# Kernel optimization log

Measured on AMD Instinct MI355X. Metric: run time of the kernel, lower is better.

## Reference

```python
import jax, jax.numpy as jnp
import numpy as np

N_NODES = 50000
N_EDGES = 800000
IN_FEAT = 128
HIDDEN = 128
N_CLASSES = 32


def setup_inputs() -> dict:
    key = jax.random.key(0)
    ks = jax.random.split(key, 8)
    x = jax.random.normal(ks[0], (N_NODES, IN_FEAT), dtype=jnp.float32)
    edge_index = jax.random.randint(ks[1], (2, N_EDGES), 0, N_NODES, dtype=jnp.int64)
    def glorot(k, fan_in, fan_out):
        s = jnp.sqrt(2.0 / (fan_in + fan_out)).astype(jnp.float32)
        return jax.random.normal(k, (fan_in, fan_out), dtype=jnp.float32) * s
    W1 = glorot(ks[2], IN_FEAT, 2 * HIDDEN)
    b1 = jnp.zeros((2 * HIDDEN,), dtype=jnp.float32)
    W2 = glorot(ks[3], 2 * HIDDEN, HIDDEN)
    b2 = jnp.zeros((HIDDEN,), dtype=jnp.float32)
    W3 = glorot(ks[4], HIDDEN, N_CLASSES)
    b3 = jnp.zeros((N_CLASSES,), dtype=jnp.float32)
    return {"x": x, "edge_index": edge_index, "W1": W1, "b1": b1,
            "W2": W2, "b2": b2, "W3": W3, "b3": b3}


def _gcn_norm(edge_index, num_nodes):
    # PyG GCNConv default: add self-loops, symmetric normalization D^-1/2 (A+I) D^-1/2
    loops = jnp.arange(num_nodes, dtype=edge_index.dtype)
    src = jnp.concatenate([edge_index[0], loops])
    dst = jnp.concatenate([edge_index[1], loops])
    ones = jnp.ones_like(dst, dtype=jnp.float32)
    deg = jax.ops.segment_sum(ones, dst, num_segments=num_nodes)
    dinv = jnp.where(deg > 0, 1.0 / jnp.sqrt(deg), 0.0)
    norm = dinv[src] * dinv[dst]  # [E + N]
    return src, dst, norm


def _gcn_conv(x, src, dst, norm, W, b, num_nodes):
    h = x @ W                               # [N, out]
    msg = h[src] * norm[:, None]            # gather + per-edge scale, [E+N, out]
    agg = jax.ops.segment_sum(msg, dst, num_segments=num_nodes)  # scatter-add
    return agg + b


def reference(x, edge_index, W1, b1, W2, b2, W3, b3):
    n = x.shape[0]
    src, dst, norm = _gcn_norm(edge_index, n)
    h = jax.nn.relu(_gcn_conv(x, src, dst, norm, W1, b1, n))
    h = jax.nn.relu(_gcn_conv(h, src, dst, norm, W2, b2, n))
    return _gcn_conv(h, src, dst, norm, W3, b3, n)
```

## Files before the change

### kernel.cpp

```cpp
#include <hip/hip_runtime.h>
#include <hip/hip_fp16.h>

#define NN 50000
#define NE 800000
#define NBKT 391
#define P1B 128

typedef __attribute__((ext_vector_type(8))) _Float16 half8v;
typedef __attribute__((ext_vector_type(4))) float f32x4;

static inline size_t align_up(size_t x, size_t a) { return (x + a - 1) & ~(a - 1); }

union U8 {
    ushort4 u;
    __half2 h[2];
};

__device__ __forceinline__ float4 u8_to_f4(ushort4 uu) {
    U8 c;
    c.u = uu;
    float2 f01 = __half22float2(c.h[0]);
    float2 f23 = __half22float2(c.h[1]);
    return make_float4(f01.x, f01.y, f23.x, f23.y);
}

__device__ __forceinline__ ushort4 f4_to_u8(float4 v) {
    U8 c;
    c.h[0] = __floats2half2_rn(v.x, v.y);
    c.h[1] = __floats2half2_rn(v.z, v.w);
    return c.u;
}

__device__ __forceinline__ int detect64(const int* __restrict__ e) {
    int ok = 1;
    for (int k = 1; k < 64; k += 2) ok &= (e[k] == 0);
    return ok;
}

__global__ __launch_bounds__(256) void bucket_hist(const int* __restrict__ e,
                                                   int* __restrict__ gcount,
                                                   int* __restrict__ base, int E) {
    __shared__ int hist[NBKT];
    const int is64 = detect64(e);
    for (int t = threadIdx.x; t < NBKT; t += 256) hist[t] = 0;
    __syncthreads();
    const int chunk = (E + P1B - 1) / P1B;
    const int b0 = blockIdx.x * chunk;
    const int b1 = min(E, b0 + chunk);
    for (int i = b0 + threadIdx.x; i < b1; i += 256) {
        int d = is64 ? e[2 * (E + i)] : e[E + i];
        atomicAdd(&hist[d >> 7], 1);
    }
    __syncthreads();
    for (int t = threadIdx.x; t < NBKT; t += 256)
        base[blockIdx.x * NBKT + t] = atomicAdd(&gcount[t], hist[t]);
}

__global__ __launch_bounds__(512) void bucket_scan(const int* __restrict__ gcount,
                                                   int* __restrict__ bstart, int nb) {
    __shared__ int s[512];
    const int t = threadIdx.x;
    int v = (t < nb) ? gcount[t] : 0;
    s[t] = v;
    __syncthreads();
    for (int off = 1; off < 512; off <<= 1) {
        int tv = (t >= off) ? s[t - off] : 0;
        __syncthreads();
        s[t] += tv;
        __syncthreads();
    }
    if (t < nb) bstart[t] = s[t] - v;
    if (t == 0) bstart[nb] = s[511];
}

__global__ __launch_bounds__(256) void bucket_scatter(const int* __restrict__ e,
                                                      const int* __restrict__ bstart,
                                                      const int* __restrict__ base,
                                                      unsigned* __restrict__ pairs, int E) {
    __shared__ int cur[NBKT];
    const int is64 = detect64(e);
    for (int t = threadIdx.x; t < NBKT; t += 256)
        cur[t] = bstart[t] + base[blockIdx.x * NBKT + t];
    __syncthreads();
    const int chunk = (E + P1B - 1) / P1B;
    const int b0 = blockIdx.x * chunk;
    const int b1 = min(E, b0 + chunk);
    for (int i = b0 + threadIdx.x; i < b1; i += 256) {
        int s = is64 ? e[2 * i] : e[i];
        int d = is64 ? e[2 * (E + i)] : e[E + i];
        int pos = atomicAdd(&cur[d >> 7], 1);
        pairs[pos] = (unsigned)s | ((unsigned)(d & 127) << 16);
    }
}

__global__ __launch_bounds__(256) void bucket_finalize(const unsigned* __restrict__ pairs,
                                                       const int* __restrict__ bstart,
                                                       const float* __restrict__ x,
                                                       int* __restrict__ row_start,
                                                       int* __restrict__ deg_cnt,
                                                       float* __restrict__ dinv,
                                                       unsigned short* __restrict__ csr,
                                                       unsigned short* __restrict__ xh, int n) {
    __shared__ int ldeg[128];
    __shared__ int lscan[128];
    __shared__ int cur[128];
    __shared__ float sdinv[128];
    const int bkt = blockIdx.x;
    const int s0 = bstart[bkt], s1 = bstart[bkt + 1];
    if (threadIdx.x < 128) ldeg[threadIdx.x] = 0;
    __syncthreads();
    for (int i = s0 + threadIdx.x; i < s1; i += 256)
        atomicAdd(&ldeg[pairs[i] >> 16], 1);
    __syncthreads();
    if (threadIdx.x < 128) lscan[threadIdx.x] = ldeg[threadIdx.x];
    __syncthreads();
    for (int off = 1; off < 128; off <<= 1) {
        int v = 0;
        if (threadIdx.x < 128 && threadIdx.x >= off) v = lscan[threadIdx.x - off];
        __syncthreads();
        if (threadIdx.x < 128) lscan[threadIdx.x] += v;
        __syncthreads();
    }
    if (threadIdx.x < 128) {
        int node = (bkt << 7) + threadIdx.x;
        int exc = s0 + lscan[threadIdx.x] - ldeg[threadIdx.x];
        cur[threadIdx.x] = exc;
        float di = rsqrtf((float)(ldeg[threadIdx.x] + 1));
        sdinv[threadIdx.x] = di;
        if (node < n) {
            row_start[node] = exc;
            deg_cnt[node] = ldeg[threadIdx.x];
            dinv[node] = di;
        }
    }
    __syncthreads();
    for (int i = s0 + threadIdx.x; i < s1; i += 256) {
        unsigned pr = pairs[i];
        int pos = atomicAdd(&cur[pr >> 16], 1);
        csr[pos] = (unsigned short)(pr & 0xFFFFu);
    }
    for (int idx = threadIdx.x; idx < 128 * 32; idx += 256) {
        int ln = idx >> 5;
        int c4 = idx & 31;
        int node = (bkt << 7) + ln;
        if (node < n) {
            float4 v = ((const float4*)x)[(size_t)node * 32 + c4];
            float s = sdinv[ln];
            v.x *= s; v.y *= s; v.z *= s; v.w *= s;
            ((ushort4*)xh)[(size_t)node * 32 + c4] = f4_to_u8(v);
        }
    }
}

__global__ void prep_weights_all(const float* __restrict__ W1, const float* __restrict__ W2,
                                 const float* __restrict__ W3,
                                 unsigned short* __restrict__ w1t,
                                 unsigned short* __restrict__ w2t,
                                 unsigned short* __restrict__ w3t,
                                 int* __restrict__ gcount) {
    int i = blockIdx.x * blockDim.x + threadIdx.x;
    if (i < NBKT + 1) gcount[i] = 0;
    const float* W;
    unsigned short* th;
    int K, M, j;
    if (i < 32768)      { W = W1; th = w1t; K = 128; M = 256; j = i; }
    else if (i < 65536) { W = W2; th = w2t; K = 256; M = 128; j = i - 32768; }
    else if (i < 69632) { W = W3; th = w3t; K = 128; M = 32;  j = i - 65536; }
    else return;
    int k = j / M, m = j % M;
    th[(size_t)m * K + k] = __half_as_ushort(__float2half_rn(W[j]));
}

template <int BM, int BN, int WM, int WN, bool BIAS, bool RELU, bool OUTF16, bool SCALE>
__global__ __launch_bounds__(256) void gemm_f16(
    const unsigned short* __restrict__ A,
    const unsigned short* __restrict__ Wt,
    const float* __restrict__ bias, const float* __restrict__ dscale,
    float* __restrict__ Cf, unsigned short* __restrict__ Ch,
    int N, int K, int M) {
    constexpr int KS = 32;
    constexpr int LDA = KS + 8;
    constexpr int WTM = BM / WM;
    constexpr int WTN = BN / WN;
    constexpr int FM = WTM / 16;
    constexpr int FN = WTN / 16;
    __shared__ unsigned short sA[BM][LDA], sW[BN][LDA];

    const int tid = threadIdx.x;
    const int lane = tid & 63;
    const int w = tid >> 6;
    const int wr = w / WN, wc = w % WN;
    const int row0 = blockIdx.y * BM;
    const int col0 = blockIdx.x * BN;

    f32x4 acc[FM][FN];
#pragma unroll
    for (int m = 0; m < FM; ++m)
#pragma unroll
        for (int nn = 0; nn < FN; ++nn) {
            f32x4 z = {0.f, 0.f, 0.f, 0.f};
            acc[m][nn] = z;
        }

    for (int k0 = 0; k0 < K; k0 += KS) {
        for (int idx = tid; idx < BM * KS / 8; idx += 256) {
            int r = idx / (KS / 8);
            int s = idx % (KS / 8);
            int gr = row0 + r;
            int4 va = make_int4(0, 0, 0, 0);
            if (gr < N) va = *(const int4*)&A[(size_t)gr * K + k0 + s * 8];
            *(int4*)&sA[r][s * 8] = va;
        }
        for (int idx = tid; idx < BN * KS / 8; idx += 256) {
            int c = idx / (KS / 8);
            int s = idx % (KS / 8);
            int gc = col0 + c;
            *(int4*)&sW[c][s * 8] = *(const int4*)&Wt[(size_t)gc * K + k0 + s * 8];
        }
        __syncthreads();

        half8v af[FM], wf[FN];
        const int koff = (lane >> 4) * 8;
        const int rsel = lane & 15;
#pragma unroll
        for (int m = 0; m < FM; ++m)
            af[m] = *(const half8v*)&sA[wr * WTM + m * 16 + rsel][koff];
#pragma unroll
        for (int nn = 0; nn < FN; ++nn)
            wf[nn] = *(const half8v*)&sW[wc * WTN + nn * 16 + rsel][koff];
#pragma unroll
        for (int m = 0; m < FM; ++m)
#pragma unroll
            for (int nn = 0; nn < FN; ++nn)
                acc[m][nn] = __builtin_amdgcn_mfma_f32_16x16x32_f16(af[m], wf[nn], acc[m][nn], 0, 0, 0);
        __syncthreads();
    }

#pragma unroll
    for (int m = 0; m < FM; ++m) {
#pragma unroll
        for (int r = 0; r < 4; ++r) {
            int row = row0 + wr * WTM + m * 16 + (lane >> 4) * 4 + r;
            if (row >= N) continue;
            float rs = SCALE ? dscale[row] : 1.f;
#pragma unroll
            for (int nn = 0; nn < FN; ++nn) {
                int col = col0 + wc * WTN + nn * 16 + (lane & 15);
                float v = acc[m][nn][r];
                if (BIAS) v += bias[col];
                if (RELU) v = fmaxf(v, 0.f);
                if (SCALE) v *= rs;
                if constexpr (OUTF16) {
                    Ch[(size_t)row * M + col] = __half_as_ushort(__float2half_rn(v));
                } else {
                    Cf[(size_t)row * M + col] = v;
                }
            }
        }
    }
}

__device__ __forceinline__ float4 add4(float4 v, float4 a) {
    a.x += v.x; a.y += v.y; a.z += v.z; a.w += v.w;
    return a;
}

template <int F, int NPB, bool BIAS, bool RELU, bool OUTF16>
__global__ __launch_bounds__((F / 4) * NPB) void agg4h(
    const unsigned short* __restrict__ h, const int* __restrict__ row_start,
    const int* __restrict__ deg_cnt, const unsigned short* __restrict__ csr,
    const float* __restrict__ dinv, const float* __restrict__ bias,
    float* __restrict__ outf, unsigned short* __restrict__ outh, int n) {
    constexpr int L = F / 4;
    const int local = threadIdx.x / L;
    const int lane = threadIdx.x % L;
    const int node = blockIdx.x * NPB + local;
    if (node >= n) return;

    const ushort4* __restrict__ h4 = (const ushort4*)h;
    const float di = dinv[node];

    float4 acc = u8_to_f4(h4[(size_t)node * L + lane]);

    const int beg = row_start[node];
    const int num = deg_cnt[node];
    int e = 0;
    for (; e + 8 <= num; e += 8) {
        int c[8];
        ushort4 raw[8];
#pragma unroll
        for (int u = 0; u < 8; ++u) c[u] = csr[beg + e + u];
#pragma unroll
        for (int u = 0; u < 8; ++u) raw[u] = h4[(size_t)c[u] * L + lane];
#pragma unroll
        for (int u = 0; u < 8; ++u) acc = add4(u8_to_f4(raw[u]), acc);
    }
    for (; e < num; ++e) {
        const int c = csr[beg + e];
        acc = add4(u8_to_f4(h4[(size_t)c * L + lane]), acc);
    }
    acc.x *= di; acc.y *= di; acc.z *= di; acc.w *= di;
    if (BIAS) {
        const float4 b = ((const float4*)bias)[lane];
        acc.x += b.x; acc.y += b.y; acc.z += b.z; acc.w += b.w;
    }
    if (RELU) {
        acc.x = fmaxf(acc.x, 0.f); acc.y = fmaxf(acc.y, 0.f);
        acc.z = fmaxf(acc.z, 0.f); acc.w = fmaxf(acc.w, 0.f);
    }
    if constexpr (OUTF16) {
        ((ushort4*)outh)[(size_t)node * L + lane] = f4_to_u8(acc);
    } else {
        ((float4*)outf)[(size_t)node * L + lane] = acc;
    }
}

extern "C" void kernel_launch(void* const* d_in, const int* in_sizes, int n_in,
                              void* d_out, int out_size, void* d_ws, size_t ws_size,
                              hipStream_t stream) {
    const float* x   = (const float*)d_in[0];
    const int*   eix = (const int*)d_in[1];
    const float* W1  = (const float*)d_in[2];
    const float* b1  = (const float*)d_in[3];
    const float* W2  = (const float*)d_in[4];
    const float* b2  = (const float*)d_in[5];
    const float* W3  = (const float*)d_in[6];
    const float* b3  = (const float*)d_in[7];
    float* out = (float*)d_out;

    const int n = NN, E = NE;

    char* p = (char*)d_ws;
    auto alloc = [&](size_t bytes) { void* r = (void*)p; p += align_up(bytes, 256); return r; };
    int*   deg_cnt   = (int*)alloc((size_t)n * 4);
    float* dinv      = (float*)alloc((size_t)n * 4);
    int*   row_start = (int*)alloc((size_t)n * 4);
    int*   gcount    = (int*)alloc((size_t)(NBKT + 1) * 4);
    int*   bstart    = (int*)alloc((size_t)(NBKT + 1) * 4);
    int*   base      = (int*)alloc((size_t)P1B * NBKT * 4);
    unsigned* pairs  = (unsigned*)alloc((size_t)E * 4);
    unsigned short* csr = (unsigned short*)alloc((size_t)E * 2);
    unsigned short* w1t = (unsigned short*)alloc((size_t)128 * 256 * 2);
    unsigned short* w2t = (unsigned short*)alloc((size_t)256 * 128 * 2);
    unsigned short* w3t = (unsigned short*)alloc((size_t)128 * 32 * 2);
    unsigned short* xh   = (unsigned short*)alloc((size_t)n * 128 * 2);
    unsigned short* agg0 = (unsigned short*)alloc((size_t)n * 128 * 2);
    unsigned short* h1   = (unsigned short*)alloc((size_t)n * 256 * 2);
    unsigned short* h2s  = (unsigned short*)alloc((size_t)n * 128 * 2);
    unsigned short* x3   = (unsigned short*)alloc((size_t)n * 128 * 2);
    unsigned short* h3s  = (unsigned short*)alloc((size_t)n * 32 * 2);
    (void)ws_size; (void)in_sizes; (void)n_in; (void)out_size;

    prep_weights_all<<<(69632 + 255) / 256, 256, 0, stream>>>(
        W1, W2, W3, w1t, w2t, w3t, gcount);

    bucket_hist<<<P1B, 256, 0, stream>>>(eix, gcount, base, E);
    bucket_scan<<<1, 512, 0, stream>>>(gcount, bstart, NBKT);
    bucket_scatter<<<P1B, 256, 0, stream>>>(eix, bstart, base, pairs, E);
    bucket_finalize<<<NBKT, 256, 0, stream>>>(pairs, bstart, x, row_start, deg_cnt,
                                              dinv, csr, xh, n);

    const int RB = (n + 127) / 128;

    agg4h<128, 8, false, false, true><<<(n + 7) / 8, 256, 0, stream>>>(
        xh, row_start, deg_cnt, csr, dinv, nullptr, nullptr, agg0, n);
    gemm_f16<128, 128, 2, 2, true, true, true, false><<<dim3(2, RB), 256, 0, stream>>>(
        agg0, w1t, b1, nullptr, nullptr, h1, n, 128, 256);

    gemm_f16<128, 128, 2, 2, false, false, true, true><<<dim3(1, RB), 256, 0, stream>>>(
        h1, w2t, nullptr, dinv, nullptr, h2s, n, 256, 128);
    agg4h<128, 8, true, true, true><<<(n + 7) / 8, 256, 0, stream>>>(
        h2s, row_start, deg_cnt, csr, dinv, b2, nullptr, x3, n);

    gemm_f16<128, 32, 4, 1, false, false, true, true><<<dim3(1, RB), 256, 0, stream>>>(
        x3, w3t, nullptr, dinv, nullptr, h3s, n, 128, 32);
    agg4h<32, 32, true, false, false><<<(n + 31) / 32, 256, 0, stream>>>(
        h3s, row_start, deg_cnt, csr, dinv, b3, out, nullptr, n);
}
```

Baseline: 177.0 us.

## Double GEMM K-step, enlarge P1B block, predicate aggregation tail into batched loop

Raises the GEMM shared-memory K tile from 32 to 64 so each barrier pair feeds two MFMA steps per fragment, halving the number of K iterations and syncs. Doubles the P1B preprocessing block size. In the aggregation kernel, the scalar remainder loop is removed: tail edges are handled inside the 8-wide batched loop by clamping indices and masking the adds, so all gathers are issued together. The costs are more LDS use per GEMM block, which may reduce occupancy, and redundant loads of the clamped neighbour for tail slots.

```diff
diff --git a/kernel.cpp b/kernel.cpp
--- a/kernel.cpp
+++ b/kernel.cpp
@@ -4,7 +4,7 @@
 #define NN 50000
 #define NE 800000
 #define NBKT 391
-#define P1B 128
+#define P1B 256
 
 typedef __attribute__((ext_vector_type(8))) _Float16 half8v;
 typedef __attribute__((ext_vector_type(4))) float f32x4;
@@ -178,7 +178,7 @@
     const float* __restrict__ bias, const float* __restrict__ dscale,
     float* __restrict__ Cf, unsigned short* __restrict__ Ch,
     int N, int K, int M) {
-    constexpr int KS = 32;
+    constexpr int KS = 64;
     constexpr int LDA = KS + 8;
     constexpr int WTM = BM / WM;
     constexpr int WTN = BN / WN;
@@ -219,20 +219,26 @@
         }
         __syncthreads();
 
-        half8v af[FM], wf[FN];
+        half8v af[FM][2], wf[FN][2];
         const int koff = (lane >> 4) * 8;
         const int rsel = lane & 15;
 #pragma unroll
+        for (int m = 0; m < FM; ++m) {
+            af[m][0] = *(const half8v*)&sA[wr * WTM + m * 16 + rsel][koff];
+            af[m][1] = *(const half8v*)&sA[wr * WTM + m * 16 + rsel][32 + koff];
+        }
+#pragma unroll
+        for (int nn = 0; nn < FN; ++nn) {
+            wf[nn][0] = *(const half8v*)&sW[wc * WTN + nn * 16 + rsel][koff];
+            wf[nn][1] = *(const half8v*)&sW[wc * WTN + nn * 16 + rsel][32 + koff];
+        }
+#pragma unroll
         for (int m = 0; m < FM; ++m)
-            af[m] = *(const half8v*)&sA[wr * WTM + m * 16 + rsel][koff];
-#pragma unroll
-        for (int nn = 0; nn < FN; ++nn)
-            wf[nn] = *(const half8v*)&sW[wc * WTN + nn * 16 + rsel][koff];
-#pragma unroll
-        for (int m = 0; m < FM; ++m)
-#pragma unroll
-            for (int nn = 0; nn < FN; ++nn)
-                acc[m][nn] = __builtin_amdgcn_mfma_f32_16x16x32_f16(af[m], wf[nn], acc[m][nn], 0, 0, 0);
+#pragma unroll
+            for (int nn = 0; nn < FN; ++nn) {
+                acc[m][nn] = __builtin_amdgcn_mfma_f32_16x16x32_f16(af[m][0], wf[nn][0], acc[m][nn], 0, 0, 0);
+                acc[m][nn] = __builtin_amdgcn_mfma_f32_16x16x32_f16(af[m][1], wf[nn][1], acc[m][nn], 0, 0, 0);
+            }
         __syncthreads();
     }
 
@@ -284,20 +290,21 @@
 
     const int beg = row_start[node];
     const int num = deg_cnt[node];
-    int e = 0;
-    for (; e + 8 <= num; e += 8) {
+    for (int e = 0; e < num; e += 8) {
         int c[8];
         ushort4 raw[8];
 #pragma unroll
-        for (int u = 0; u < 8; ++u) c[u] = csr[beg + e + u];
+        for (int u = 0; u < 8; ++u) {
+            int idx = min(e + u, num - 1);
+            c[u] = csr[beg + idx];
+        }
 #pragma unroll
         for (int u = 0; u < 8; ++u) raw[u] = h4[(size_t)c[u] * L + lane];
 #pragma unroll
-        for (int u = 0; u < 8; ++u) acc = add4(u8_to_f4(raw[u]), acc);
-    }
-    for (; e < num; ++e) {
-        const int c = csr[beg + e];
-        acc = add4(u8_to_f4(h4[(size_t)c * L + lane]), acc);
+        for (int u = 0; u < 8; ++u) {
+            float4 v = u8_to_f4(raw[u]);
+            if (e + u < num) acc = add4(v, acc);
+        }
     }
     acc.x *= di; acc.y *= di; acc.z *= di; acc.w *= di;
     if (BIAS) {
```

Result: no change. 174.6 us (-1.3%).
